# Kernel tuning notes

Hardware: AMD Instinct MI355X
Metric: run time of the kernel (lower is better)

The kernel has to match this reference:

```python
import jax, jax.numpy as jnp
import numpy as np

NUM_GROUPS = 50
ALPHA = 2.0  # epoch=1, alpha_step=50 -> alpha never incremented


def setup_inputs() -> dict:
    key = jax.random.key(0)
    k1, k2, k3, k4 = jax.random.split(key, 4)
    B, C, N = 2, 64, 8192
    l0_points = jax.random.normal(k1, (B, C, N), dtype=jnp.float32)
    W = jax.random.normal(k2, (3, C), dtype=jnp.float32) * 0.1  # conv2_1 1x1 kernel
    b = jax.random.normal(k3, (3,), dtype=jnp.float32) * 0.1
    target = jax.random.randint(k4, (B, N), 0, NUM_GROUPS, dtype=jnp.int64)
    return {"l0_points": l0_points, "W": W, "b": b, "target": target}


def reference(l0_points, W, b, target):
    # Fsim = conv2_1(l0_points) : 1x1 conv == channel matmul. [B, 3, N]
    Fsim = jnp.einsum("oc,bcn->bon", W, l0_points) + b[None, :, None]
    # pairwise squared euclidean distance matrix D[b,i,j] = ||f_i - f_j||^2
    r = jnp.sum(Fsim * Fsim, axis=1)  # [B, N]
    mul = 2.0 * jnp.einsum("bcn,bcm->bnm", Fsim, Fsim)  # [B, N, N]
    D = r[:, None, :] - mul + r[:, :, None]
    D = jnp.maximum(D, 0.0)  # D[D <= 0] = 0
    # group one-hot (labels == -1 masked out)
    valid = (target != -1)[..., None].astype(D.dtype)
    one_hot = jax.nn.one_hot(target, NUM_GROUPS, dtype=D.dtype) * valid  # [B, N, G]
    same = jnp.einsum("bng,bmg->bnm", one_hot, one_hot)  # [B, N, N]
    N = same.shape[1]
    eye = jnp.eye(N, dtype=bool)
    same = jnp.where(eye[None, :, :], 1.0, same)  # diag forced to 1
    diff = 1.0 - same
    inv_sq = 1.0 / ((D + 1.0) * (D + 1.0))
    simmat_loss = 100.0 * (ALPHA * diff * inv_sq + same * D)
    return jnp.mean(simmat_loss)
```

## Files before the change

### kernel.cpp

```cpp
#include <hip/hip_runtime.h>

#define NPTS    8192
#define BATCH   2
#define CH      64
#define NGROUPS 50

#define TS      256
#define NROW    (NPTS/TS)
#define NTILEB  (NROW*(NROW+1)/2)
#define MAINPB  (NTILEB*2)
#define MAINB   (BATCH*MAINPB)
#define NBUCK   (BATCH*NGROUPS)
#define CORRB   (NBUCK*4)
#define GRID_T  (CORRB+MAINB)
#define PAD     256

__global__ __launch_bounds__(256) void fsim_kernel(
    const float* __restrict__ l0, const float* __restrict__ W,
    const float* __restrict__ bias, const int* __restrict__ target,
    float* __restrict__ fx, float* __restrict__ fy, float* __restrict__ fz,
    float* __restrict__ fw, int* __restrict__ gidx, int* __restrict__ gcnt)
{
    const int bid = blockIdx.x, tid = threadIdx.x;

    if (bid < 256) {
        __shared__ float sW[3 * CH];
        if (tid < 3 * CH) sW[tid] = W[tid];
        __syncthreads();
        const int lane = tid & 63, wave = tid >> 6;
        const int p = lane & 15, cg = lane >> 4;
        const int pt = bid * 64 + wave * 16 + p;
        const int b = pt >> 13, n = pt & (NPTS - 1);
        const float* basep = l0 + (size_t)b * CH * NPTS + n;
        float ax = 0.f, ay = 0.f, az = 0.f;
        #pragma unroll
        for (int k = 0; k < 16; ++k) {
            int c = cg * 16 + k;
            float v = basep[(size_t)c * NPTS];
            ax = fmaf(sW[c], v, ax);
            ay = fmaf(sW[CH + c], v, ay);
            az = fmaf(sW[2*CH + c], v, az);
        }
        ax += __shfl_down(ax,32,64); ay += __shfl_down(ay,32,64); az += __shfl_down(az,32,64);
        ax += __shfl_down(ax,16,64); ay += __shfl_down(ay,16,64); az += __shfl_down(az,16,64);
        if (cg == 0) {
            float X = ax + bias[0], Y = ay + bias[1], Z = az + bias[2];
            fx[pt] = X; fy[pt] = Y; fz[pt] = Z;
            fw[pt] = fmaf(X, X, fmaf(Y, Y, Z * Z));
        }
    } else {
        const int bucket = bid - 256;
        const int b = bucket / NGROUPS, L = bucket % NGROUPS;
        const int tbase = b * NPTS;
        __shared__ int scnt[256];
        int cnt = 0;
        const int4* t4 = (const int4*)&target[tbase];
        #pragma unroll
        for (int k8 = 0; k8 < 8; ++k8) {
            int4 tv = t4[tid * 8 + k8];
            cnt += (tv.x == L) + (tv.y == L) + (tv.z == L) + (tv.w == L);
        }
        scnt[tid] = cnt;
        __syncthreads();
        for (int s = 1; s < 256; s <<= 1) {
            int a = (tid >= s) ? scnt[tid - s] : 0;
            __syncthreads();
            scnt[tid] += a;
            __syncthreads();
        }
        int wpos = scnt[tid] - cnt;
        for (int k = 0; k < 32; ++k) {
            int idx = tid * 32 + k;
            if (target[tbase + idx] == L) {
                if (wpos < PAD) gidx[bucket * PAD + wpos] = idx;
                ++wpos;
            }
        }
        if (tid == 0) gcnt[bucket] = min(scnt[255], PAD);
    }
}

#define PAIR4(QX, QY, QZ, QP)                          \
    { _Pragma("unroll")                                \
      for (int u = 0; u < 4; ++u) {                    \
        float t = si[u] + (QP);                        \
        t = fmaf(nx[u], (QX), t);                      \
        t = fmaf(ny[u], (QY), t);                      \
        t = fmaf(nz[u], (QZ), t);                      \
        float r = __builtin_amdgcn_rcpf(t);            \
        acc[u] = fmaf(r, r, acc[u]);                   \
      } }

__global__ __launch_bounds__(256) void pair_kernel(
    const float* __restrict__ fx, const float* __restrict__ fy,
    const float* __restrict__ fz, const float* __restrict__ fw,
    const int* __restrict__ gidx, const int* __restrict__ gcnt,
    double* __restrict__ partials)
{
    const int bid = blockIdx.x, tid = threadIdx.x;
    __shared__ float4 sj[PAD];
    __shared__ double wsum[4];

    float  accv = 0.0f;
    double cadd = 0.0;

    if (bid >= CORRB) {
        const int mid = bid - CORRB;
        const int b   = mid / MAINPB;
        const int r   = mid % MAINPB;
        const int tau = r >> 1, half = r & 1;
        int ti = (int)(32.5f - sqrtf(32.5f * 32.5f - 2.0f * (float)tau));
        if (ti < 0) ti = 0; if (ti > NROW - 1) ti = NROW - 1;
        while ((ti + 1) * (65 - (ti + 1)) / 2 <= tau) ++ti;
        while (ti * (65 - ti) / 2 > tau) --ti;
        const int tj = ti + (tau - ti * (65 - ti) / 2);

        const int base = b * NPTS;
        const int ib = base + ti * TS + (tid & 63) * 4;
        const float4 vx = *(const float4*)&fx[ib];
        const float4 vy = *(const float4*)&fy[ib];
        const float4 vz = *(const float4*)&fz[ib];
        const float4 vw = *(const float4*)&fw[ib];
        const float nx[4] = {-2.f*vx.x, -2.f*vx.y, -2.f*vx.z, -2.f*vx.w};
        const float ny[4] = {-2.f*vy.x, -2.f*vy.y, -2.f*vy.z, -2.f*vy.w};
        const float nz[4] = {-2.f*vz.x, -2.f*vz.y, -2.f*vz.z, -2.f*vz.w};
        const float si[4] = {vw.x+1.f, vw.y+1.f, vw.z+1.f, vw.w+1.f};

        if (tid < 128) {
            const int k = base + tj * TS + half * 128 + tid;
            sj[tid] = make_float4(fx[k], fy[k], fz[k], fw[k]);
        }
        __syncthreads();

        const int j0 = (tid >> 6) * 32;
        float acc[4] = {0.f, 0.f, 0.f, 0.f};
        #pragma unroll 4
        for (int jj = 0; jj < 32; ++jj) {
            float4 q = sj[j0 + jj];
            PAIR4(q.x, q.y, q.z, q.w)
        }
        float s = (acc[0] + acc[1]) + (acc[2] + acc[3]);
        accv = (ti == tj) ? (2.0f * s) : (4.0f * s);
    } else {
        const int bucket = bid >> 2, sub = bid & 3;
        const int b = bucket / NGROUPS;
        const int cnt = gcnt[bucket];
        const int base = b * NPTS;
        {
            float4 pv = make_float4(0.f, 0.f, 0.f, 0.f);
            if (tid < cnt) {
                int ix = base + gidx[bucket * PAD + tid];
                pv = make_float4(fx[ix], fy[ix], fz[ix], 1.0f);
            }
            sj[tid] = pv;
        }
        __syncthreads();
        const int pp = sub * 64 + (tid & 63);
        const int g0 = (tid >> 6) * 64;
        if (pp < cnt) {
            const float4 a = sj[pp];
            float accB = 0.f;
            #pragma unroll 4
            for (int qq = g0; qq < g0 + 64; ++qq) {
                float4 c = sj[qq];
                float dx = a.x - c.x, dy = a.y - c.y, dz = a.z - c.z;
                float t = fmaf(dx, dx, fmaf(dy, dy, fmaf(dz, dz, 1.0f)));
                float rr = __builtin_amdgcn_rcpf(t); rr = rr * rr;
                accB = fmaf(fmaf(-2.0f, rr, t), c.w, accB);
            }
            accv = accB;
        }
        if (sub == 0 && tid == 0) {
            double c = (double)cnt;
            cadd = 2.0 * c - c * c;
        }
    }

    #pragma unroll
    for (int o = 32; o > 0; o >>= 1) accv += __shfl_down(accv, o, 64);
    if ((tid & 63) == 0) wsum[tid >> 6] = (double)accv;
    __syncthreads();
    if (tid == 0)
        partials[bid] = (wsum[0] + wsum[1]) + (wsum[2] + wsum[3]) + cadd;
}

__global__ __launch_bounds__(256) void finalize_kernel(
    const double* __restrict__ partials, float* __restrict__ out)
{
    const int tid = threadIdx.x;
    double s = 0.0;
    for (int k = tid; k < GRID_T; k += 256) s += partials[k];
    #pragma unroll
    for (int o = 32; o > 0; o >>= 1) s += __shfl_down(s, o, 64);
    __shared__ double sd[4];
    if ((tid & 63) == 0) sd[tid >> 6] = s;
    __syncthreads();
    if (tid == 0) {
        double tot = (sd[0] + sd[1]) + (sd[2] + sd[3]);
        tot -= 2.0 * (double)(BATCH * NPTS);
        out[0] = (float)(100.0 * tot / ((double)BATCH * NPTS * NPTS));
    }
}

extern "C" void kernel_launch(void* const* d_in, const int* in_sizes, int n_in,
                              void* d_out, int out_size, void* d_ws, size_t ws_size,
                              hipStream_t stream) {
    const float* l0     = (const float*)d_in[0];
    const float* W      = (const float*)d_in[1];
    const float* bias   = (const float*)d_in[2];
    const int*   target = (const int*)d_in[3];
    float* out = (float*)d_out;

    float* fx = (float*)d_ws;
    float* fy = fx + BATCH * NPTS;
    float* fz = fy + BATCH * NPTS;
    float* fw = fz + BATCH * NPTS;
    double* partials = (double*)((char*)d_ws + 4 * BATCH * NPTS * sizeof(float));
    int* gidx = (int*)((char*)partials + GRID_T * sizeof(double));
    int* gcnt = gidx + NBUCK * PAD;

    fsim_kernel<<<256 + NBUCK, 256, 0, stream>>>(l0, W, bias, target,
                                                 fx, fy, fz, fw, gidx, gcnt);
    pair_kernel<<<GRID_T, 256, 0, stream>>>(fx, fy, fz, fw, gidx, gcnt, partials);
    finalize_kernel<<<1, 256, 0, stream>>>(partials, out);
}
```

Baseline: 33.10 us.

## Pack features as float4 AoS, fold correction work into main blocks, read j-tiles from global

Stores per-point features as one interleaved float4 array instead of four separate planes. The pair kernel now runs only the main tile blocks: the first CORRB blocks do the same-group correction and then also do a main tile, so the grid shrinks. The j-points are read directly from global memory at a wave-uniform address (readfirstlane) rather than staged through shared memory. This is meant to cut block count, tail imbalance and shared-memory syncs. In exchange it relies on scalar or cached global loads for the j-stream and makes the blocks that carry correction work longer.

```diff
diff --git a/kernel.cpp b/kernel.cpp
--- a/kernel.cpp
+++ b/kernel.cpp
@@ -6,20 +6,18 @@
 #define NGROUPS 50
 
 #define TS      256
-#define NROW    (NPTS/TS)
+#define NROW    32
 #define NTILEB  (NROW*(NROW+1)/2)
 #define MAINPB  (NTILEB*2)
 #define MAINB   (BATCH*MAINPB)
 #define NBUCK   (BATCH*NGROUPS)
 #define CORRB   (NBUCK*4)
-#define GRID_T  (CORRB+MAINB)
 #define PAD     256
 
 __global__ __launch_bounds__(256) void fsim_kernel(
     const float* __restrict__ l0, const float* __restrict__ W,
     const float* __restrict__ bias, const int* __restrict__ target,
-    float* __restrict__ fx, float* __restrict__ fy, float* __restrict__ fz,
-    float* __restrict__ fw, int* __restrict__ gidx, int* __restrict__ gcnt)
+    float4* __restrict__ fj4, int* __restrict__ gidx, int* __restrict__ gcnt)
 {
     const int bid = blockIdx.x, tid = threadIdx.x;
 
@@ -45,8 +43,7 @@
         ax += __shfl_down(ax,16,64); ay += __shfl_down(ay,16,64); az += __shfl_down(az,16,64);
         if (cg == 0) {
             float X = ax + bias[0], Y = ay + bias[1], Z = az + bias[2];
-            fx[pt] = X; fy[pt] = Y; fz[pt] = Z;
-            fw[pt] = fmaf(X, X, fmaf(Y, Y, Z * Z));
+            fj4[pt] = make_float4(X, Y, Z, fmaf(X, X, fmaf(Y, Y, Z * Z)));
         }
     } else {
         const int bucket = bid - 256;
@@ -80,20 +77,8 @@
     }
 }
 
-#define PAIR4(QX, QY, QZ, QP)                          \
-    { _Pragma("unroll")                                \
-      for (int u = 0; u < 4; ++u) {                    \
-        float t = si[u] + (QP);                        \
-        t = fmaf(nx[u], (QX), t);                      \
-        t = fmaf(ny[u], (QY), t);                      \
-        t = fmaf(nz[u], (QZ), t);                      \
-        float r = __builtin_amdgcn_rcpf(t);            \
-        acc[u] = fmaf(r, r, acc[u]);                   \
-      } }
-
 __global__ __launch_bounds__(256) void pair_kernel(
-    const float* __restrict__ fx, const float* __restrict__ fy,
-    const float* __restrict__ fz, const float* __restrict__ fw,
+    const float4* __restrict__ fj4,
     const int* __restrict__ gidx, const int* __restrict__ gcnt,
     double* __restrict__ partials)
 {
@@ -104,44 +89,7 @@
     float  accv = 0.0f;
     double cadd = 0.0;
 
-    if (bid >= CORRB) {
-        const int mid = bid - CORRB;
-        const int b   = mid / MAINPB;
-        const int r   = mid % MAINPB;
-        const int tau = r >> 1, half = r & 1;
-        int ti = (int)(32.5f - sqrtf(32.5f * 32.5f - 2.0f * (float)tau));
-        if (ti < 0) ti = 0; if (ti > NROW - 1) ti = NROW - 1;
-        while ((ti + 1) * (65 - (ti + 1)) / 2 <= tau) ++ti;
-        while (ti * (65 - ti) / 2 > tau) --ti;
-        const int tj = ti + (tau - ti * (65 - ti) / 2);
-
-        const int base = b * NPTS;
-        const int ib = base + ti * TS + (tid & 63) * 4;
-        const float4 vx = *(const float4*)&fx[ib];
-        const float4 vy = *(const float4*)&fy[ib];
-        const float4 vz = *(const float4*)&fz[ib];
-        const float4 vw = *(const float4*)&fw[ib];
-        const float nx[4] = {-2.f*vx.x, -2.f*vx.y, -2.f*vx.z, -2.f*vx.w};
-        const float ny[4] = {-2.f*vy.x, -2.f*vy.y, -2.f*vy.z, -2.f*vy.w};
-        const float nz[4] = {-2.f*vz.x, -2.f*vz.y, -2.f*vz.z, -2.f*vz.w};
-        const float si[4] = {vw.x+1.f, vw.y+1.f, vw.z+1.f, vw.w+1.f};
-
-        if (tid < 128) {
-            const int k = base + tj * TS + half * 128 + tid;
-            sj[tid] = make_float4(fx[k], fy[k], fz[k], fw[k]);
-        }
-        __syncthreads();
-
-        const int j0 = (tid >> 6) * 32;
-        float acc[4] = {0.f, 0.f, 0.f, 0.f};
-        #pragma unroll 4
-        for (int jj = 0; jj < 32; ++jj) {
-            float4 q = sj[j0 + jj];
-            PAIR4(q.x, q.y, q.z, q.w)
-        }
-        float s = (acc[0] + acc[1]) + (acc[2] + acc[3]);
-        accv = (ti == tj) ? (2.0f * s) : (4.0f * s);
-    } else {
+    if (bid < CORRB) {
         const int bucket = bid >> 2, sub = bid & 3;
         const int b = bucket / NGROUPS;
         const int cnt = gcnt[bucket];
@@ -149,8 +97,8 @@
         {
             float4 pv = make_float4(0.f, 0.f, 0.f, 0.f);
             if (tid < cnt) {
-                int ix = base + gidx[bucket * PAD + tid];
-                pv = make_float4(fx[ix], fy[ix], fz[ix], 1.0f);
+                float4 g = fj4[base + gidx[bucket * PAD + tid]];
+                pv = make_float4(g.x, g.y, g.z, 1.0f);
             }
             sj[tid] = pv;
         }
@@ -174,6 +122,47 @@
             double c = (double)cnt;
             cadd = 2.0 * c - c * c;
         }
+        __syncthreads();
+    }
+
+    {
+        const int b   = bid / MAINPB;
+        const int r   = bid % MAINPB;
+        const int tau = r >> 1, half = r & 1;
+        int ti = (int)(32.5f - sqrtf(32.5f * 32.5f - 2.0f * (float)tau));
+        if (ti < 0) ti = 0; if (ti > NROW - 1) ti = NROW - 1;
+        while ((ti + 1) * (65 - (ti + 1)) / 2 <= tau) ++ti;
+        while (ti * (65 - ti) / 2 > tau) --ti;
+        const int tj = ti + (tau - ti * (65 - ti) / 2);
+
+        const int base = b * NPTS;
+        const int ib = base + ti * TS + (tid & 63) * 4;
+        const float4 p0 = fj4[ib + 0], p1 = fj4[ib + 1];
+        const float4 p2 = fj4[ib + 2], p3 = fj4[ib + 3];
+        const float nx[4] = {-2.f*p0.x, -2.f*p1.x, -2.f*p2.x, -2.f*p3.x};
+        const float ny[4] = {-2.f*p0.y, -2.f*p1.y, -2.f*p2.y, -2.f*p3.y};
+        const float nz[4] = {-2.f*p0.z, -2.f*p1.z, -2.f*p2.z, -2.f*p3.z};
+        const float si[4] = {p0.w+1.f, p1.w+1.f, p2.w+1.f, p3.w+1.f};
+
+        const int jb = __builtin_amdgcn_readfirstlane(
+                           base + tj * TS + half * 128 + (tid >> 6) * 32);
+
+        float acc[4] = {0.f, 0.f, 0.f, 0.f};
+        #pragma unroll 8
+        for (int jj = 0; jj < 32; ++jj) {
+            const float4 q = fj4[jb + jj];
+            #pragma unroll
+            for (int u = 0; u < 4; ++u) {
+                float t = si[u] + q.w;
+                t = fmaf(nx[u], q.x, t);
+                t = fmaf(ny[u], q.y, t);
+                t = fmaf(nz[u], q.z, t);
+                float rcp = __builtin_amdgcn_rcpf(t);
+                acc[u] = fmaf(rcp, rcp, acc[u]);
+            }
+        }
+        float s = (acc[0] + acc[1]) + (acc[2] + acc[3]);
+        accv += (ti == tj) ? (2.0f * s) : (4.0f * s);
     }
 
     #pragma unroll
@@ -189,7 +178,7 @@
 {
     const int tid = threadIdx.x;
     double s = 0.0;
-    for (int k = tid; k < GRID_T; k += 256) s += partials[k];
+    for (int k = tid; k < MAINB; k += 256) s += partials[k];
     #pragma unroll
     for (int o = 32; o > 0; o >>= 1) s += __shfl_down(s, o, 64);
     __shared__ double sd[4];
@@ -211,16 +200,12 @@
     const int*   target = (const int*)d_in[3];
     float* out = (float*)d_out;
 
-    float* fx = (float*)d_ws;
-    float* fy = fx + BATCH * NPTS;
-    float* fz = fy + BATCH * NPTS;
-    float* fw = fz + BATCH * NPTS;
-    double* partials = (double*)((char*)d_ws + 4 * BATCH * NPTS * sizeof(float));
-    int* gidx = (int*)((char*)partials + GRID_T * sizeof(double));
-    int* gcnt = gidx + NBUCK * PAD;
-
-    fsim_kernel<<<256 + NBUCK, 256, 0, stream>>>(l0, W, bias, target,
-                                                 fx, fy, fz, fw, gidx, gcnt);
-    pair_kernel<<<GRID_T, 256, 0, stream>>>(fx, fy, fz, fw, gidx, gcnt, partials);
+    float4* fj4      = (float4*)d_ws;
+    double* partials = (double*)((char*)d_ws + BATCH * NPTS * sizeof(float4));
+    int*    gidx     = (int*)((char*)partials + MAINB * sizeof(double));
+    int*    gcnt     = gidx + NBUCK * PAD;
+
+    fsim_kernel<<<256 + NBUCK, 256, 0, stream>>>(l0, W, bias, target, fj4, gidx, gcnt);
+    pair_kernel<<<MAINB, 256, 0, stream>>>(fj4, gidx, gcnt, partials);
     finalize_kernel<<<1, 256, 0, stream>>>(partials, out);
 }
```

Result: slower. 34.27 us (+3.5%).
